# Kernel optimization log

Hardware: AMD Instinct MI355X
Metric: run time of the kernel (lower is better)

The kernel has to match this reference:

```python
import jax, jax.numpy as jnp
import numpy as np

NUM_HEAD = 16


def setup_inputs() -> dict:
    key = jax.random.key(0)
    ks = jax.random.split(key, 4)
    B, C, D = 2, 2048, 1024
    hidden_states = jax.random.normal(ks[0], (B, C, D), dtype=jnp.float32)
    attention_mask = jnp.zeros((B, 1, C, C), dtype=jnp.float32)
    Wqkv = jax.random.normal(ks[1], (D, 3 * D), dtype=jnp.float32) * (D ** -0.5)
    bqkv = jnp.zeros((3 * D,), dtype=jnp.float32)
    Wo = jax.random.normal(ks[2], (D, D), dtype=jnp.float32) * (D ** -0.5)
    bo = jnp.zeros((D,), dtype=jnp.float32)
    return {"hidden_states": hidden_states, "attention_mask": attention_mask,
            "Wqkv": Wqkv, "bqkv": bqkv, "Wo": Wo, "bo": bo}


def reference(hidden_states, attention_mask, Wqkv, bqkv, Wo, bo):
    B, C, D = hidden_states.shape
    H = NUM_HEAD
    hd = D // H
    scaling = hd ** -0.5

    qkv = hidden_states @ Wqkv + bqkv                      # [B, C, 3D]
    q, k, v = jnp.split(qkv, 3, axis=-1)
    # [B, C, H, hd] -> [B, H, C, hd]
    q = q.reshape(B, C, H, hd).transpose(0, 2, 1, 3)
    k = k.reshape(B, C, H, hd).transpose(0, 2, 1, 3)
    v = v.reshape(B, C, H, hd).transpose(0, 2, 1, 3)

    scores = jnp.einsum("bhqd,bhkd->bhqk", q, k) * scaling  # [B, H, C, C]
    causal = jnp.tril(jnp.ones((C, C), dtype=bool))[None, None]
    mask = jnp.where(causal, attention_mask, -jnp.inf)      # [B, 1, C, C]
    probs = jax.nn.softmax(scores + mask, axis=-1)
    out = jnp.einsum("bhqk,bhkd->bhqd", probs, v)           # [B, H, C, hd]
    out = out.transpose(0, 2, 1, 3).reshape(B, C, D)
    return out @ Wo + bo
```

## Files before the change

kernel.cpp:

```cpp
#include <hip/hip_runtime.h>
#include <hip/hip_bf16.h>
#include <cstdint>
#include <cstddef>

typedef __attribute__((ext_vector_type(8))) short short8;
typedef __attribute__((ext_vector_type(4))) float f32x4;
typedef __attribute__((ext_vector_type(16))) float f32x16;
typedef __attribute__((ext_vector_type(4))) unsigned int u32x4;
typedef unsigned short u16;
typedef unsigned int u32;

#define B_ 2
#define C_ 2048
#define D_ 1024
#define H_ 16
#define HD_ 64
#define LOG2E 1.4426950408889634f

static __device__ __forceinline__ u16 f2b(float f) {
  u32 x = __builtin_bit_cast(u32, f);
  x += 0x7FFFu + ((x >> 16) & 1u);
  return (u16)(x >> 16);
}
static __device__ __forceinline__ float b2f(u16 v) {
  return __builtin_bit_cast(float, (u32)v << 16);
}

__device__ const unsigned char SEGTAB[20] = {
  1, 66, 67, 83, 132, 148, 133, 149, 165, 198, 214, 230, 199, 215, 231, 247,
  0, 82, 164, 246};

__global__ void k_convert(const float* __restrict__ in, u16* __restrict__ out, int n) {
  int i = (blockIdx.x * blockDim.x + threadIdx.x) * 4;
  const int stride = gridDim.x * blockDim.x * 4;
  for (; i < n; i += stride) {
    float4 v = *reinterpret_cast<const float4*>(in + i);
    ushort4 o;
    o.x = f2b(v.x); o.y = f2b(v.y); o.z = f2b(v.z); o.w = f2b(v.w);
    *reinterpret_cast<ushort4*>(out + i) = o;
  }
}

__global__ void k_tconv(const float* __restrict__ in, u16* __restrict__ out, int R, int Cc) {
  __shared__ float tile[64][65];
  const int tC = blockIdx.x * 64;
  const int tR = blockIdx.y * 64;
  const int t = threadIdx.x;
  const int r0 = t >> 4;
  const int c0 = (t & 15) * 4;
#pragma unroll
  for (int ii = 0; ii < 4; ++ii) {
    int r = ii * 16 + r0;
    float4 v = *reinterpret_cast<const float4*>(&in[(size_t)(tR + r) * Cc + tC + c0]);
    tile[r][c0] = v.x; tile[r][c0 + 1] = v.y; tile[r][c0 + 2] = v.z; tile[r][c0 + 3] = v.w;
  }
  __syncthreads();
#pragma unroll
  for (int ii = 0; ii < 4; ++ii) {
    int c = ii * 16 + r0;
    ushort4 o;
    o.x = f2b(tile[c0 + 0][c]);
    o.y = f2b(tile[c0 + 1][c]);
    o.z = f2b(tile[c0 + 2][c]);
    o.w = f2b(tile[c0 + 3][c]);
    *reinterpret_cast<ushort4*>(&out[(size_t)(tC + c) * R + tR + c0]) = o;
  }
}

__global__ void k_maskflags(const float* __restrict__ mask, u32* __restrict__ flags) {
  const int bid = blockIdx.x;
  const int kt = bid & 31, qs = (bid >> 5) & 31, b = bid >> 10;
  const int t = threadIdx.x;
  const float* base = mask + ((size_t)b * C_ + qs * 64) * C_ + kt * 64;
  const int row = t >> 2, c0 = (t & 3) * 16;
  int any = 0;
#pragma unroll
  for (int i = 0; i < 4; ++i) {
    float4 v = *reinterpret_cast<const float4*>(base + (size_t)row * C_ + c0 + i * 4);
    any |= (v.x != 0.f) | (v.y != 0.f) | (v.z != 0.f) | (v.w != 0.f);
  }
  __shared__ int sh[4];
  const unsigned long long bal = __ballot(any);
  if ((t & 63) == 0) sh[t >> 6] = (bal != 0ull);
  __syncthreads();
  if (t == 0) flags[bid] = (u32)(sh[0] | sh[1] | sh[2] | sh[3]);
}

#define GLL16(gptr, lptr) __builtin_amdgcn_global_load_lds( \
    (const __attribute__((address_space(1))) u32*)(gptr),   \
    (__attribute__((address_space(3))) u32*)(lptr), 16, 0, 0)

template<int EPI, int BM>
__global__ __launch_bounds__(256) void k_gemm(
    const u16* __restrict__ A, const u16* __restrict__ Bt,
    int M, int N, int K, const float* __restrict__ bias,
    u16* __restrict__ Cq, u16* __restrict__ Ck, u16* __restrict__ Cv,
    float* __restrict__ Cf)
{
  constexpr int WCW = (BM == 128) ? 64 : 32;
  constexpr int NF = WCW / 16;
  __shared__ __align__(16) u16 As[BM * 64];
  __shared__ __align__(16) u16 Bs[128 * 64];
  const int t = threadIdx.x;
  const int l = t & 63, w = t >> 6;
  const int wr = (BM == 128) ? (w >> 1) : 0;
  const int wc = (BM == 128) ? (w & 1) : w;
  const int lr = l & 15, lg = l >> 4;
  const int swk = lr & 7;
  const int m0 = blockIdx.y * BM, n0 = blockIdx.x * 128;
  f32x4 acc[4][NF] = {};

  for (int k0 = 0; k0 < K; k0 += 64) {
#pragma unroll
    for (int s = 0; s < BM / 32; ++s) {
      const int u = s * 256 + t;
      const int row = u >> 3, slot = (u & 7) ^ (row & 7);
      GLL16(A + (size_t)(m0 + row) * K + k0 + (slot << 3), As + (u << 3));
    }
#pragma unroll
    for (int s = 0; s < 4; ++s) {
      const int u = s * 256 + t;
      const int row = u >> 3, slot = (u & 7) ^ (row & 7);
      GLL16(Bt + (size_t)(n0 + row) * K + k0 + (slot << 3), Bs + (u << 3));
    }
    __syncthreads();
    short8 af[2][4], bfr[2][NF];
#pragma unroll
    for (int s = 0; s < 2; ++s) {
#pragma unroll
      for (int m = 0; m < 4; ++m)
        af[s][m] = *reinterpret_cast<const short8*>(
            &As[((wr * 64 + m * 16 + lr) << 6) + (((s * 4 + lg) ^ swk) << 3)]);
#pragma unroll
      for (int n = 0; n < NF; ++n)
        bfr[s][n] = *reinterpret_cast<const short8*>(
            &Bs[((wc * WCW + n * 16 + lr) << 6) + (((s * 4 + lg) ^ swk) << 3)]);
    }
#pragma unroll
    for (int s = 0; s < 2; ++s)
#pragma unroll
      for (int m = 0; m < 4; ++m)
#pragma unroll
        for (int n = 0; n < NF; ++n)
          acc[m][n] = __builtin_amdgcn_mfma_f32_16x16x32_bf16(af[s][m], bfr[s][n], acc[m][n], 0, 0, 0);
    __syncthreads();
  }

#pragma unroll
  for (int m = 0; m < 4; ++m) {
    const int mg = m0 + wr * 64 + m * 16 + lg * 4;
    const int bq = mg >> 11, c0 = mg & 2047;
#pragma unroll
    for (int n = 0; n < NF; ++n) {
      const int ng = n0 + wc * WCW + n * 16 + lr;
      const float bia = bias[ng];
      if (EPI == 0) {
        const int reg = ng >> 10, d = ng & 1023, h = d >> 6, e = d & 63;
        if (reg == 2) {
          u16* vp = Cv + (((size_t)(bq * H_ + h) * HD_ + e) << 11) + c0;
#pragma unroll
          for (int j = 0; j < 4; ++j) vp[j] = f2b(acc[m][n][j] + bia);
        } else {
          u16* dst = (reg == 0) ? Cq : Ck;
#pragma unroll
          for (int j = 0; j < 4; ++j)
            dst[(((size_t)(bq * H_ + h) * C_ + c0 + j) << 6) + e] = f2b(acc[m][n][j] + bia);
        }
      } else {
#pragma unroll
        for (int j = 0; j < 4; ++j)
          Cf[(size_t)(mg + j) * N + ng] = acc[m][n][j] + bia;
      }
    }
  }
}

static __device__ __forceinline__ void stage_kv(
    const u16* __restrict__ Kbh, const u16* __restrict__ Vbh,
    u16* Kd, u16* Vd, int kt, int t)
{
  const int row = t >> 3, slot = (t & 7) ^ (row & 7);
  GLL16(Kbh + (((size_t)(kt * 64 + row)) << 6) + (slot << 3), Kd + (t << 3));
  GLL16(Vbh + (((size_t)row) << 11) + kt * 64 + (slot << 3), Vd + (t << 3));
}

__global__ __launch_bounds__(512) void k_attn(
    const u16* __restrict__ Q, const u16* __restrict__ Kb, const u16* __restrict__ Vt,
    const float* __restrict__ mask, const u32* __restrict__ flags,
    u16* __restrict__ O, u16* __restrict__ Opart, float2* __restrict__ ml)
{
  __shared__ __align__(16) u16 buf[16384];
  u16* const Klb = buf;
  u16* const Vlb = buf + 8192;
  const int bid = blockIdx.x;
  const int bh = bid & 31;
  const int e = SEGTAB[bid >> 5];
  const int qt = e & 15, seg = (e >> 4) & 3, nseg = (e >> 6) + 1;
  const int ntiles = 4 * qt + 4;
  const int kt0 = seg * 8;
  const int kt1 = (kt0 + 8 < ntiles) ? kt0 + 8 : ntiles;
  const int slotbase = (qt < 4) ? (qt - 2) * 2
                     : (qt < 6) ? 4 + (qt - 4) * 3
                     : 10 + (qt - 6) * 4;
  const int slot = bh * 18 + slotbase + seg;

  const int b = bh >> 4, h = bh & 15;
  const int t = threadIdx.x;
  const int l = t & 63, w = t >> 6;
  const int q = l & 31, hi = l >> 5;
  const int q7 = q & 7;

  const u16* Kbh = Kb + (size_t)bh * (C_ * HD_);
  const u16* Vbh = Vt + (size_t)bh * (HD_ * C_);

  const int q0w = qt * 256 + w * 32;
  const int qg = q0w + q;
  const int qmaxw = q0w + 31;

  short8 aq[4];
  {
    const u16* qp = Q + ((size_t)bh * C_ + qg) * HD_ + hi * 8;
#pragma unroll
    for (int kh = 0; kh < 4; ++kh) {
      short8 v = *reinterpret_cast<const short8*>(qp + kh * 16);
#pragma unroll
      for (int i = 0; i < 8; ++i) {
        const float f = b2f((u16)v[i]) * (0.125f * LOG2E);
        v[i] = (short)f2b(f);
      }
      aq[kh] = v;
    }
  }

  f32x16 oa0 = {}, oa1 = {};
  float mrun = -INFINITY, srun = 0.f;
  const float* mrow = mask + ((size_t)b * C_ + qg) * C_;
  const u32* fb = flags + (size_t)(b * 32 + (q0w >> 6)) * 32;

  stage_kv(Kbh, Vbh, Klb, Vlb, kt0, t);

#pragma unroll 1
  for (int kt = kt0; kt < kt1; ++kt) {
    const int cur = kt & 1;
    __syncthreads();
    if (kt + 1 < kt1) stage_kv(Kbh, Vbh, Klb + (cur ^ 1) * 4096, Vlb + (cur ^ 1) * 4096,
                               kt + 1, t);
    if (kt * 64 > qmaxw) continue;

    const char* Kc = reinterpret_cast<const char*>(Klb + cur * 4096);
    const char* Vc = reinterpret_cast<const char*>(Vlb + cur * 4096);

    f32x16 p0 = {}, p1 = {};
#pragma unroll
    for (int kh = 0; kh < 4; ++kh) {
      const int sl = ((2 * kh + hi) ^ q7) << 4;
      const short8 k0 = *reinterpret_cast<const short8*>(Kc + q * 128 + sl);
      const short8 k1 = *reinterpret_cast<const short8*>(Kc + (32 + q) * 128 + sl);
      p0 = __builtin_amdgcn_mfma_f32_32x32x16_bf16(k0, aq[kh], p0, 0, 0, 0);
      p1 = __builtin_amdgcn_mfma_f32_32x32x16_bf16(k1, aq[kh], p1, 0, 0, 0);
    }

    if (fb[kt]) {
      const float* mp = mrow + kt * 64 + 4 * hi;
#pragma unroll
      for (int g = 0; g < 4; ++g) {
        const float4 m0 = *reinterpret_cast<const float4*>(mp + 8 * g);
        const float4 m1 = *reinterpret_cast<const float4*>(mp + 32 + 8 * g);
        p0[4*g+0] = fmaf(m0.x, LOG2E, p0[4*g+0]);
        p0[4*g+1] = fmaf(m0.y, LOG2E, p0[4*g+1]);
        p0[4*g+2] = fmaf(m0.z, LOG2E, p0[4*g+2]);
        p0[4*g+3] = fmaf(m0.w, LOG2E, p0[4*g+3]);
        p1[4*g+0] = fmaf(m1.x, LOG2E, p1[4*g+0]);
        p1[4*g+1] = fmaf(m1.y, LOG2E, p1[4*g+1]);
        p1[4*g+2] = fmaf(m1.z, LOG2E, p1[4*g+2]);
        p1[4*g+3] = fmaf(m1.w, LOG2E, p1[4*g+3]);
      }
    }
    if (kt * 64 + 63 > q0w) {
#pragma unroll
      for (int r = 0; r < 16; ++r) {
        const int kl = kt * 64 + (r & 3) + 8 * (r >> 2) + 4 * hi;
        if (kl > qg) p0[r] = -INFINITY;
        if (kl + 32 > qg) p1[r] = -INFINITY;
      }
    }

    float pm = -INFINITY;
#pragma unroll
    for (int r = 0; r < 16; ++r) pm = fmaxf(pm, fmaxf(p0[r], p1[r]));
    pm = fmaxf(pm, __shfl_xor(pm, 32));
    if (__ballot(pm > mrun) != 0ull) {
      const float mn = fmaxf(fmaxf(mrun, pm), -1e30f);
      const float rs = exp2f(mrun - mn);
      srun *= rs;
      oa0 *= rs; oa1 *= rs;
      mrun = mn;
    }
    float sum = 0.f;
#pragma unroll
    for (int r = 0; r < 16; ++r) {
      p0[r] = exp2f(p0[r] - mrun); sum += p0[r];
      p1[r] = exp2f(p1[r] - mrun); sum += p1[r];
    }
    sum += __shfl_xor(sum, 32);
    srun += sum;

    __builtin_amdgcn_s_setprio(1);
#pragma unroll
    for (int ks = 0; ks < 4; ++ks) {
      const int o = (ks & 1) * 8;
      u32 X, X2, Y, Y2;
      if (ks < 2) {
        asm("v_cvt_pk_bf16_f32 %0, %1, %2" : "=v"(X)  : "v"(p0[o+0]), "v"(p0[o+1]));
        asm("v_cvt_pk_bf16_f32 %0, %1, %2" : "=v"(X2) : "v"(p0[o+2]), "v"(p0[o+3]));
        asm("v_cvt_pk_bf16_f32 %0, %1, %2" : "=v"(Y)  : "v"(p0[o+4]), "v"(p0[o+5]));
        asm("v_cvt_pk_bf16_f32 %0, %1, %2" : "=v"(Y2) : "v"(p0[o+6]), "v"(p0[o+7]));
      } else {
        asm("v_cvt_pk_bf16_f32 %0, %1, %2" : "=v"(X)  : "v"(p1[o+0]), "v"(p1[o+1]));
        asm("v_cvt_pk_bf16_f32 %0, %1, %2" : "=v"(X2) : "v"(p1[o+2]), "v"(p1[o+3]));
        asm("v_cvt_pk_bf16_f32 %0, %1, %2" : "=v"(Y)  : "v"(p1[o+4]), "v"(p1[o+5]));
        asm("v_cvt_pk_bf16_f32 %0, %1, %2" : "=v"(Y2) : "v"(p1[o+6]), "v"(p1[o+7]));
      }
      asm("v_permlane32_swap_b32 %0, %1" : "+v"(X), "+v"(Y));
      asm("v_permlane32_swap_b32 %0, %1" : "+v"(X2), "+v"(Y2));
      const u32x4 bw = {X, X2, Y, Y2};
      const short8 bp = __builtin_bit_cast(short8, bw);
      const int sl = ((2 * ks + hi) ^ q7) << 4;
      const short8 v0 = *reinterpret_cast<const short8*>(Vc + q * 128 + sl);
      const short8 v1 = *reinterpret_cast<const short8*>(Vc + (32 + q) * 128 + sl);
      oa0 = __builtin_amdgcn_mfma_f32_32x32x16_bf16(v0, bp, oa0, 0, 0, 0);
      oa1 = __builtin_amdgcn_mfma_f32_32x32x16_bf16(v1, bp, oa1, 0, 0, 0);
    }
    __builtin_amdgcn_s_setprio(0);
  }

  const float rinv = 1.f / srun;
  const int q2 = l >> 1, hf = l & 1;
#pragma unroll 1
  for (int ph = 0; ph < 2; ++ph) {
    __syncthreads();
    if ((w >> 2) == ph) {
      char* Swb = reinterpret_cast<char*>(buf) + (w & 3) * 4608;
#pragma unroll
      for (int g = 0; g < 4; ++g) {
        const int d0 = 8 * g + 4 * hi;
        const float a0 = oa0[4*g+0] * rinv, a1 = oa0[4*g+1] * rinv;
        const float a2 = oa0[4*g+2] * rinv, a3 = oa0[4*g+3] * rinv;
        const float b0 = oa1[4*g+0] * rinv, b1 = oa1[4*g+1] * rinv;
        const float b2 = oa1[4*g+2] * rinv, b3 = oa1[4*g+3] * rinv;
        u32 w0, w1, w2, w3;
        asm("v_cvt_pk_bf16_f32 %0, %1, %2" : "=v"(w0) : "v"(a0), "v"(a1));
        asm("v_cvt_pk_bf16_f32 %0, %1, %2" : "=v"(w1) : "v"(a2), "v"(a3));
        asm("v_cvt_pk_bf16_f32 %0, %1, %2" : "=v"(w2) : "v"(b0), "v"(b1));
        asm("v_cvt_pk_bf16_f32 %0, %1, %2" : "=v"(w3) : "v"(b2), "v"(b3));
        *reinterpret_cast<uint2*>(Swb + q * 144 + d0 * 2) = make_uint2(w0, w1);
        *reinterpret_cast<uint2*>(Swb + q * 144 + (d0 + 32) * 2) = make_uint2(w2, w3);
      }
      asm volatile("" ::: "memory");
      if (nseg == 1) {
        u16* orow = O + ((size_t)b * C_ + q0w + q2) * D_ + h * 64 + hf * 32;
#pragma unroll
        for (int i = 0; i < 4; ++i) {
          const short8 v = *reinterpret_cast<const short8*>(Swb + q2 * 144 + hf * 64 + i * 16);
          *reinterpret_cast<short8*>(orow + i * 8) = v;
        }
      } else {
        u16* prow = Opart + (((size_t)slot * 256 + w * 32 + q2) << 6) + hf * 32;
#pragma unroll
        for (int i = 0; i < 4; ++i) {
          const short8 v = *reinterpret_cast<const short8*>(Swb + q2 * 144 + hf * 64 + i * 16);
          *reinterpret_cast<short8*>(prow + i * 8) = v;
        }
      }
    }
  }
  if (nseg > 1 && hi == 0)
    ml[(size_t)slot * 256 + w * 32 + q] = make_float2(mrun, srun);
}

__global__ __launch_bounds__(512) void k_merge(
    const u16* __restrict__ Opart, const float2* __restrict__ ml, u16* __restrict__ O)
{
  const int bid = blockIdx.x;
  const int bh = bid & 31;
  const int qt = 2 + (bid >> 5);
  const int nseg = (qt < 4) ? 2 : (qt < 6) ? 3 : 4;
  const int slotbase = (qt < 4) ? (qt - 2) * 2
                     : (qt < 6) ? 4 + (qt - 4) * 3
                     : 10 + (qt - 6) * 4;
  const int slot0 = bh * 18 + slotbase;
  const int b = bh >> 4, h = bh & 15;
  const int t = threadIdx.x;
  const int q = t >> 1, dh = t & 1;

  float m[4], l_[4];
  float M = -INFINITY;
#pragma unroll 4
  for (int s = 0; s < nseg; ++s) {
    const float2 v = ml[(size_t)(slot0 + s) * 256 + q];
    m[s] = v.x; l_[s] = v.y;
    M = fmaxf(M, v.x);
  }
  float a[4], L = 0.f;
#pragma unroll 4
  for (int s = 0; s < nseg; ++s) { a[s] = exp2f(m[s] - M) * l_[s]; L += a[s]; }
  const float rL = 1.f / L;

  float acc[32] = {};
#pragma unroll 4
  for (int s = 0; s < nseg; ++s) {
    const u16* op = Opart + (((size_t)(slot0 + s) * 256 + q) << 6) + dh * 32;
    const float ws = a[s] * rL;
#pragma unroll
    for (int i = 0; i < 4; ++i) {
      const short8 v = *reinterpret_cast<const short8*>(op + i * 8);
#pragma unroll
      for (int j = 0; j < 8; ++j) acc[i * 8 + j] += ws * b2f((u16)v[j]);
    }
  }
  u16* orow = O + ((size_t)b * C_ + qt * 256 + q) * D_ + h * 64 + dh * 32;
#pragma unroll
  for (int i = 0; i < 4; ++i) {
    short8 v;
#pragma unroll
    for (int j = 0; j < 8; ++j) v[j] = (short)f2b(acc[i * 8 + j]);
    *reinterpret_cast<short8*>(orow + i * 8) = v;
  }
}

extern "C" void kernel_launch(void* const* d_in, const int* in_sizes, int n_in,
                              void* d_out, int out_size, void* d_ws, size_t ws_size,
                              hipStream_t stream) {
  const float* hs   = (const float*)d_in[0];
  const float* mask = (const float*)d_in[1];
  const float* Wqkv = (const float*)d_in[2];
  const float* bqkv = (const float*)d_in[3];
  const float* Wo   = (const float*)d_in[4];
  const float* bo   = (const float*)d_in[5];
  float* out = (float*)d_out;
  char* ws = (char*)d_ws;

  u16*    hsb   = (u16*)(ws);
  u16*    Opart = (u16*)(ws);
  u16*    Wqkvt = (u16*)(ws + (8  << 20));
  float2* mlbuf = (float2*)(ws + (19 << 20));
  u32*    flags = (u32*)(ws + (20 << 20) + (1 << 19));
  u16*    Wot   = (u16*)(ws + (21 << 20));
  u16*    Qb    = (u16*)(ws + (24 << 20));
  u16*    Kb    = (u16*)(ws + (32 << 20));
  u16*    Vtb   = (u16*)(ws + (40 << 20));
  u16*    AOb   = (u16*)(ws + (48 << 20));

  k_convert<<<2048, 256, 0, stream>>>(hs, hsb, 4096 * 1024);
  k_tconv<<<dim3(3072 / 64, 1024 / 64), 256, 0, stream>>>(Wqkv, Wqkvt, 1024, 3072);
  k_tconv<<<dim3(1024 / 64, 1024 / 64), 256, 0, stream>>>(Wo, Wot, 1024, 1024);
  k_maskflags<<<2048, 256, 0, stream>>>(mask, flags);
  k_gemm<0, 128><<<dim3(24, 32), 256, 0, stream>>>(hsb, Wqkvt, 4096, 3072, 1024, bqkv,
                                                   Qb, Kb, Vtb, nullptr);
  k_attn<<<640, 512, 0, stream>>>(Qb, Kb, Vtb, mask, flags, AOb, Opart, mlbuf);
  k_merge<<<192, 512, 0, stream>>>(Opart, mlbuf, AOb);
  k_gemm<1, 64><<<dim3(8, 64), 256, 0, stream>>>(AOb, Wot, 4096, 1024, 1024, bo,
                                                 nullptr, nullptr, nullptr, out);
}
```

Baseline: 137.0 us.

## Triple-buffer K/V LDS staging with explicit vmcnt waits, prefetch two tiles ahead

Moves the attention kernel's K/V staging from a double buffer to a triple buffer, so two tiles are prefetched ahead. Each iteration now waits with an explicit s_waitcnt vmcnt and a raw s_barrier instead of __syncthreads, which lets the prefetch of tile kt+1 stay in flight while tile kt is computed. The per-tile mask flags are also loaded once into a bitmask up front, removing a global load from each iteration. In exchange LDS use per block rises from 32KB to 48KB, and correctness now depends on the hand-counted vmcnt matching the number of async loads issued per stage.

```diff
diff --git a/kernel.cpp b/kernel.cpp
--- a/kernel.cpp
+++ b/kernel.cpp
@@ -189,9 +189,7 @@
     const float* __restrict__ mask, const u32* __restrict__ flags,
     u16* __restrict__ O, u16* __restrict__ Opart, float2* __restrict__ ml)
 {
-  __shared__ __align__(16) u16 buf[16384];
-  u16* const Klb = buf;
-  u16* const Vlb = buf + 8192;
+  __shared__ __align__(16) u16 buf[3 * 8192];
   const int bid = blockIdx.x;
   const int bh = bid & 31;
   const int e = SEGTAB[bid >> 5];
@@ -232,23 +230,35 @@
     }
   }
 
+  u32 fbits = 0;
+  {
+    const u32* fp = flags + (size_t)(b * 32 + (q0w >> 6)) * 32 + kt0;
+#pragma unroll
+    for (int i = 0; i < 8; ++i) fbits |= (fp[i] ? 1u : 0u) << i;
+  }
+
   f32x16 oa0 = {}, oa1 = {};
   float mrun = -INFINITY, srun = 0.f;
   const float* mrow = mask + ((size_t)b * C_ + qg) * C_;
-  const u32* fb = flags + (size_t)(b * 32 + (q0w >> 6)) * 32;
-
-  stage_kv(Kbh, Vbh, Klb, Vlb, kt0, t);
+
+  stage_kv(Kbh, Vbh, buf, buf + 4096, kt0, t);
+  if (kt0 + 1 < kt1) stage_kv(Kbh, Vbh, buf + 8192, buf + 8192 + 4096, kt0 + 1, t);
 
 #pragma unroll 1
   for (int kt = kt0; kt < kt1; ++kt) {
-    const int cur = kt & 1;
-    __syncthreads();
-    if (kt + 1 < kt1) stage_kv(Kbh, Vbh, Klb + (cur ^ 1) * 4096, Vlb + (cur ^ 1) * 4096,
-                               kt + 1, t);
+    const int bi = (kt - kt0) % 3;
+    if (kt + 1 < kt1) asm volatile("s_waitcnt vmcnt(2)" ::: "memory");
+    else              asm volatile("s_waitcnt vmcnt(0)" ::: "memory");
+    __builtin_amdgcn_s_barrier();
+    __builtin_amdgcn_sched_barrier(0);
+    if (kt + 2 < kt1) {
+      const int bn = (kt + 2 - kt0) % 3;
+      stage_kv(Kbh, Vbh, buf + bn * 8192, buf + bn * 8192 + 4096, kt + 2, t);
+    }
     if (kt * 64 > qmaxw) continue;
 
-    const char* Kc = reinterpret_cast<const char*>(Klb + cur * 4096);
-    const char* Vc = reinterpret_cast<const char*>(Vlb + cur * 4096);
+    const char* Kc = reinterpret_cast<const char*>(buf + bi * 8192);
+    const char* Vc = reinterpret_cast<const char*>(buf + bi * 8192 + 4096);
 
     f32x16 p0 = {}, p1 = {};
 #pragma unroll
@@ -260,7 +270,7 @@
       p1 = __builtin_amdgcn_mfma_f32_32x32x16_bf16(k1, aq[kh], p1, 0, 0, 0);
     }
 
-    if (fb[kt]) {
+    if ((fbits >> (kt - kt0)) & 1u) {
       const float* mp = mrow + kt * 64 + 4 * hi;
 #pragma unroll
       for (int g = 0; g < 4; ++g) {
```

Result: no change. 136.7 us (-0.3%).
